# Kernel tuning notes

Measured on AMD Instinct MI355X. Metric: run time of the kernel, lower is better.

## Reference

```python
import jax, jax.numpy as jnp
import numpy as np

N, E, D = 100000, 1600000, 128      # nodes, edges, in_channels = MLP out_dim
L = 3                               # num GIN layers
OC = D + L * D                      # concat width = 512
CH, CHID = 4, 256                   # num ChannelMLPs, their hidden dim


def setup_inputs() -> dict:
    key = jax.random.key(0)
    ks = jax.random.split(key, 10)
    s = lambda fan_in: 1.0 / np.sqrt(fan_in)
    x = jax.random.normal(ks[0], (N, D), dtype=jnp.float32)
    edge_index = jax.random.randint(ks[1], (2, E), 0, N, dtype=jnp.int32)
    # conv MLPs: per layer 3 linear layers (in->hid, hid->hid, hid->out), all 128x128
    convW = jax.random.normal(ks[2], (L, 3, D, D), dtype=jnp.float32) * s(D)
    convB = jnp.zeros((L, 3, D), dtype=jnp.float32)
    # channel MLPs: 512 -> 256 -> 256 -> 1, ReLU after every layer (output_activation='relu')
    chanW1 = jax.random.normal(ks[3], (CH, OC, CHID), dtype=jnp.float32) * s(OC)
    chanB1 = jnp.zeros((CH, CHID), dtype=jnp.float32)
    chanW2 = jax.random.normal(ks[4], (CH, CHID, CHID), dtype=jnp.float32) * s(CHID)
    chanB2 = jnp.zeros((CH, CHID), dtype=jnp.float32)
    chanW3 = jax.random.normal(ks[5], (CH, CHID, 1), dtype=jnp.float32) * s(CHID)
    chanB3 = jnp.zeros((CH, 1), dtype=jnp.float32)
    return {"x": x, "edge_index": edge_index, "convW": convW, "convB": convB,
            "chanW1": chanW1, "chanB1": chanB1, "chanW2": chanW2, "chanB2": chanB2,
            "chanW3": chanW3, "chanB3": chanB3}


def reference(x, edge_index, convW, convB, chanW1, chanB1, chanW2, chanB2, chanW3, chanB3):
    src, dst = edge_index[0], edge_index[1]
    n = x.shape[0]
    feats = [x]                      # skip_first_features=False -> keep input
    h = x
    for l in range(L):
        # GINConv, eps=0: mlp((1+eps)*h + sum_{j in N(i)} h_j)
        agg = jax.ops.segment_sum(h[src], dst, num_segments=n)  # scatter-add at targets
        h = h + agg
        for k in range(3):           # MLP: Lin+ReLU x3 (2 hidden + relu output activation)
            h = jax.nn.relu(h @ convW[l, k] + convB[l, k])
        feats.append(h)
    xcat = jnp.concatenate(feats, axis=1)                       # [N, 512]
    # channel MLPs vectorized over the channel axis c
    h1 = jax.nn.relu(jnp.einsum('nd,cdh->cnh', xcat, chanW1) + chanB1[:, None, :])
    h2 = jax.nn.relu(jnp.einsum('cnh,chk->cnk', h1, chanW2) + chanB2[:, None, :])
    h3 = jax.nn.relu(jnp.einsum('cnh,cho->cno', h2, chanW3) + chanB3[:, None, :])
    return jnp.transpose(h3[..., 0])                            # [N, num_ChannelMLPs]
```

## Files before the change

### kernel.cpp

```cpp
#include <hip/hip_runtime.h>
#include <hip/hip_bf16.h>

#define D 128
#define NLAYER 3
#define NCH 4

typedef __attribute__((ext_vector_type(8))) short short8;
typedef __attribute__((ext_vector_type(4))) float f32x4;

__device__ __forceinline__ ushort f2bf(float f) {
    unsigned int u = __builtin_bit_cast(unsigned int, f);
    u += 0x7fffu + ((u >> 16) & 1u);
    return (ushort)(u >> 16);
}
__device__ __forceinline__ float bflo(unsigned int u) {
    return __builtin_bit_cast(float, u << 16);
}
__device__ __forceinline__ float bfhi(unsigned int u) {
    return __builtin_bit_cast(float, u & 0xffff0000u);
}

__global__ void hist_kernel(const int* __restrict__ dst, int* __restrict__ deg, int E) {
    int e = blockIdx.x * 256 + threadIdx.x;
    if (e < E) atomicAdd(&deg[dst[e]], 1);
}

__global__ __launch_bounds__(256) void blocksum_kernel(
    const int* __restrict__ deg, int* __restrict__ bsum, int n)
{
    int i = blockIdx.x * 256 + threadIdx.x;
    int v = (i < n) ? deg[i] : 0;
#pragma unroll
    for (int o = 1; o < 64; o <<= 1) v += __shfl_xor(v, o);
    __shared__ int s[4];
    if ((threadIdx.x & 63) == 0) s[threadIdx.x >> 6] = v;
    __syncthreads();
    if (threadIdx.x == 0) bsum[blockIdx.x] = s[0] + s[1] + s[2] + s[3];
}

__global__ __launch_bounds__(512) void scanblk_kernel(
    const int* __restrict__ bsum, int* __restrict__ boff, int nb,
    int* __restrict__ offs, int n, int E)
{
    __shared__ int sh[512];
    int t = threadIdx.x;
    sh[t] = (t < nb) ? bsum[t] : 0;
    __syncthreads();
    for (int d = 1; d < 512; d <<= 1) {
        int v = (t >= d) ? sh[t - d] : 0;
        __syncthreads();
        sh[t] += v;
        __syncthreads();
    }
    if (t < nb) boff[t] = (t == 0) ? 0 : sh[t - 1];
    if (t == 0) offs[n] = E;
}

__global__ __launch_bounds__(256) void blockscan_kernel(
    const int* __restrict__ deg, const int* __restrict__ boff,
    int* __restrict__ offs, int* __restrict__ cursor, int n)
{
    __shared__ int sh[256];
    int t = threadIdx.x;
    int i = blockIdx.x * 256 + t;
    int v = (i < n) ? deg[i] : 0;
    sh[t] = v;
    __syncthreads();
    for (int d = 1; d < 256; d <<= 1) {
        int u = (t >= d) ? sh[t - d] : 0;
        __syncthreads();
        sh[t] += u;
        __syncthreads();
    }
    if (i < n) {
        int ex = boff[blockIdx.x] + sh[t] - v;
        offs[i] = ex; cursor[i] = ex;
    }
}

#define FILL_CHUNK 4096
__global__ __launch_bounds__(256) void fill_part_kernel(
    const int* __restrict__ src, const int* __restrict__ dst,
    int* __restrict__ cursor, int* __restrict__ csr,
    int E, int nPer, int N)
{
    int cls = blockIdx.x & 7;
    int base = (blockIdx.x >> 3) * FILL_CHUNK;
    int lo = cls * nPer;
    int hi = lo + nPer; if (hi > N) hi = N;
    int end = base + FILL_CHUNK; if (end > E) end = E;
    for (int e = base + threadIdx.x; e < end; e += 256) {
        int d = dst[e];
        int s = src[e];
        if (d >= lo && d < hi) {
            int p = atomicAdd(&cursor[d], 1);
            csr[p] = s;
        }
    }
}

__global__ __launch_bounds__(256) void cvtx_kernel(
    const float* __restrict__ x, ushort* __restrict__ xb, int total8)
{
    int i = blockIdx.x * 256 + threadIdx.x;
    if (i >= total8) return;
    const float* gp = x + (size_t)i * 8;
    float4 v0 = *(const float4*)gp;
    float4 v1 = *(const float4*)(gp + 4);
    short8 pk;
    pk[0] = (short)f2bf(v0.x); pk[1] = (short)f2bf(v0.y);
    pk[2] = (short)f2bf(v0.z); pk[3] = (short)f2bf(v0.w);
    pk[4] = (short)f2bf(v1.x); pk[5] = (short)f2bf(v1.y);
    pk[6] = (short)f2bf(v1.z); pk[7] = (short)f2bf(v1.w);
    *(short8*)(xb + (size_t)i * 8) = pk;
}

__global__ void cvtW_kernel(const float* __restrict__ W, ushort* __restrict__ Wt,
                            int K, int Ncols) {
    __shared__ float tile[32][33];
    int c = blockIdx.z;
    int k0 = blockIdx.x * 32, n0 = blockIdx.y * 32;
    const float* Wc = W + (size_t)c * K * Ncols;
    ushort* Wtc = Wt + (size_t)c * K * Ncols;
    int tx = threadIdx.x & 31, ty = threadIdx.x >> 5;
#pragma unroll
    for (int i = 0; i < 4; ++i) {
        int k = k0 + ty + i * 8;
        tile[ty + i * 8][tx] = Wc[(size_t)k * Ncols + n0 + tx];
    }
    __syncthreads();
#pragma unroll
    for (int i = 0; i < 4; ++i) {
        int n = n0 + ty + i * 8;
        Wtc[(size_t)n * K + k0 + tx] = f2bf(tile[tx][ty + i * 8]);
    }
}

__global__ __launch_bounds__(256) void agg_bf16(
    const ushort* __restrict__ h,
    const int* __restrict__ offs, const int* __restrict__ csr,
    ushort* __restrict__ outb, int n)
{
    int wid = (blockIdx.x * 256 + threadIdx.x) >> 6;
    int lane = threadIdx.x & 63;
    if (wid >= n) return;
    const unsigned int* hb = (const unsigned int*)h;
    unsigned int u = hb[(size_t)wid * 64 + lane];
    float ax = bflo(u), ay = bfhi(u);
    int b = offs[wid], e = offs[wid + 1];
    int j = b;
    for (; j + 4 <= e; j += 4) {
        int s0 = csr[j], s1 = csr[j + 1], s2 = csr[j + 2], s3 = csr[j + 3];
        unsigned int u0 = hb[(size_t)s0 * 64 + lane];
        unsigned int u1 = hb[(size_t)s1 * 64 + lane];
        unsigned int u2 = hb[(size_t)s2 * 64 + lane];
        unsigned int u3 = hb[(size_t)s3 * 64 + lane];
        ax += (bflo(u0) + bflo(u1)) + (bflo(u2) + bflo(u3));
        ay += (bfhi(u0) + bfhi(u1)) + (bfhi(u2) + bfhi(u3));
    }
    for (; j < e; ++j) {
        unsigned int u0 = hb[(size_t)csr[j] * 64 + lane];
        ax += bflo(u0); ay += bfhi(u0);
    }
    unsigned int po = (unsigned int)f2bf(ax) | ((unsigned int)f2bf(ay) << 16);
    ((unsigned int*)outb)[(size_t)wid * 64 + lane] = po;
}

__global__ __launch_bounds__(256) void gin_mlp_mfma(
    const ushort* __restrict__ A,
    const ushort* __restrict__ WtL,
    const float* __restrict__ biasL,
    ushort* __restrict__ Out,
    int nrows)
{
    __shared__ __align__(16) ushort As[128 * 128];
    __shared__ __align__(16) ushort Bs[128 * 128];
    const int t = threadIdx.x;
    const int w = t >> 6, lane = t & 63;
    const int quad = lane >> 4, c15 = lane & 15;
    const int wr = w >> 1, wc = w & 1;
    const int rowbase = blockIdx.x * 128;

#pragma unroll
    for (int i = 0; i < 8; ++i) {
        int lin = (i * 4 + w) * 64 + lane;
        int row = lin >> 4, slot = lin & 15, g = slot ^ (row & 15);
        int grow = rowbase + row;
        if (grow >= nrows) grow = 0;
        const ushort* gp = A + (size_t)grow * 128 + g * 8;
        __builtin_amdgcn_global_load_lds(
            (const __attribute__((address_space(1))) void*)gp,
            (__attribute__((address_space(3))) void*)&As[(i * 4 + w) * 512],
            16, 0, 0);
    }
#pragma unroll
    for (int i = 0; i < 8; ++i) {
        int lin = (i * 4 + w) * 64 + lane;
        int n = lin >> 4, slot = lin & 15, g = slot ^ (n & 15);
        const ushort* gp = WtL + (size_t)n * 128 + g * 8;
        __builtin_amdgcn_global_load_lds(
            (const __attribute__((address_space(1))) void*)gp,
            (__attribute__((address_space(3))) void*)&Bs[(i * 4 + w) * 512],
            16, 0, 0);
    }
    __syncthreads();

    for (int s = 0; s < 3; ++s) {
        f32x4 acc[4][4];
#pragma unroll
        for (int i = 0; i < 4; ++i)
#pragma unroll
            for (int j = 0; j < 4; ++j)
#pragma unroll
                for (int r = 0; r < 4; ++r) acc[i][j][r] = 0.f;

#pragma unroll
        for (int ks = 0; ks < 4; ++ks) {
            short8 af[4], bf[4];
#pragma unroll
            for (int tr = 0; tr < 4; ++tr) {
                int r = wr * 64 + tr * 16 + c15;
                af[tr] = *(const short8*)&As[r * 128 + (((ks * 4 + quad) ^ (r & 15)) * 8)];
            }
#pragma unroll
            for (int tc = 0; tc < 4; ++tc) {
                int n = wc * 64 + tc * 16 + c15;
                bf[tc] = *(const short8*)&Bs[n * 128 + (((ks * 4 + quad) ^ (n & 15)) * 8)];
            }
#pragma unroll
            for (int tr = 0; tr < 4; ++tr)
#pragma unroll
                for (int tc = 0; tc < 4; ++tc)
                    acc[tr][tc] = __builtin_amdgcn_mfma_f32_16x16x32_bf16(
                        af[tr], bf[tc], acc[tr][tc], 0, 0, 0);
        }
        __syncthreads();

        if (s < 2) {
#pragma unroll
            for (int tc = 0; tc < 4; ++tc) {
                int col = wc * 64 + tc * 16 + c15;
                float bv = biasL[s * 128 + col];
#pragma unroll
                for (int tr = 0; tr < 4; ++tr)
#pragma unroll
                    for (int rg = 0; rg < 4; ++rg) {
                        int row = wr * 64 + tr * 16 + quad * 4 + rg;
                        As[row * 128 + (((col >> 3) ^ (row & 15)) * 8) + (col & 7)]
                            = f2bf(fmaxf(acc[tr][tc][rg] + bv, 0.f));
                    }
            }
            const ushort* Wn = WtL + (size_t)(s + 1) * 128 * 128;
#pragma unroll
            for (int i = 0; i < 8; ++i) {
                int lin = (i * 4 + w) * 64 + lane;
                int n = lin >> 4, slot = lin & 15, g = slot ^ (n & 15);
                const ushort* gp = Wn + (size_t)n * 128 + g * 8;
                __builtin_amdgcn_global_load_lds(
                    (const __attribute__((address_space(1))) void*)gp,
                    (__attribute__((address_space(3))) void*)&Bs[(i * 4 + w) * 512],
                    16, 0, 0);
            }
            __syncthreads();
        } else {
#pragma unroll
            for (int tc = 0; tc < 4; ++tc) {
                int col = wc * 64 + tc * 16 + c15;
                float bv = biasL[2 * 128 + col];
#pragma unroll
                for (int tr = 0; tr < 4; ++tr)
#pragma unroll
                    for (int rg = 0; rg < 4; ++rg) {
                        int grow = rowbase + wr * 64 + tr * 16 + quad * 4 + rg;
                        if (grow < nrows)
                            Out[(size_t)grow * 128 + col]
                                = f2bf(fmaxf(acc[tr][tc][rg] + bv, 0.f));
                    }
            }
        }
    }
}

__global__ __launch_bounds__(256, 2) void chan_l1_mfma(
    const ushort* __restrict__ A0, const ushort* __restrict__ A1,
    const ushort* __restrict__ A2, const ushort* __restrict__ A3,
    const ushort* __restrict__ WtAll,
    const float* __restrict__ b1all,
    ushort* __restrict__ T1,
    int r0, int rows, int N)
{
    __shared__ __align__(16) ushort As[128 * 64];
    __shared__ __align__(16) ushort Bs[256 * 64];
    const int t = threadIdx.x;
    const int w = t >> 6, lane = t & 63;
    const int quad = lane >> 4, c15 = lane & 15;
    const int wr = w >> 1, wc = w & 1;
    const int rowbase = blockIdx.x * 128;
    const int colbase = blockIdx.y * 256;
    const ushort* Asrc[4] = {A0, A1, A2, A3};

    f32x4 acc[4][8];
#pragma unroll
    for (int i = 0; i < 4; ++i)
#pragma unroll
        for (int j = 0; j < 8; ++j)
#pragma unroll
            for (int r = 0; r < 4; ++r) acc[i][j][r] = 0.f;

    for (int kc = 0; kc < 512; kc += 64) {
        const ushort* Ab = Asrc[kc >> 7];
        const int within = kc & 127;
#pragma unroll
        for (int i = 0; i < 4; ++i) {
            int lin = (i * 4 + w) * 64 + lane;
            int row = lin >> 3, slot = lin & 7, g = slot ^ (row & 7);
            int grow = r0 + rowbase + row;
            if (grow >= N) grow = r0;
            const ushort* gp = Ab + (size_t)grow * 128 + within + g * 8;
            __builtin_amdgcn_global_load_lds(
                (const __attribute__((address_space(1))) void*)gp,
                (__attribute__((address_space(3))) void*)&As[(i * 4 + w) * 512],
                16, 0, 0);
        }
#pragma unroll
        for (int i = 0; i < 8; ++i) {
            int lin = (i * 4 + w) * 64 + lane;
            int n = lin >> 3, slot = lin & 7, g = slot ^ (n & 7);
            const ushort* gp = WtAll + (size_t)(colbase + n) * 512 + kc + g * 8;
            __builtin_amdgcn_global_load_lds(
                (const __attribute__((address_space(1))) void*)gp,
                (__attribute__((address_space(3))) void*)&Bs[(i * 4 + w) * 512],
                16, 0, 0);
        }
        __syncthreads();
#pragma unroll
        for (int ks = 0; ks < 2; ++ks) {
            const int K8 = ks * 4;
            short8 af[4], bf[8];
#pragma unroll
            for (int tr = 0; tr < 4; ++tr) {
                int r = wr * 64 + tr * 16 + c15;
                af[tr] = *(const short8*)&As[r * 64 + (((K8 + quad) ^ (r & 7)) * 8)];
            }
#pragma unroll
            for (int tc = 0; tc < 8; ++tc) {
                int n = wc * 128 + tc * 16 + c15;
                bf[tc] = *(const short8*)&Bs[n * 64 + (((K8 + quad) ^ (n & 7)) * 8)];
            }
#pragma unroll
            for (int tr = 0; tr < 4; ++tr)
#pragma unroll
                for (int tc = 0; tc < 8; ++tc)
                    acc[tr][tc] = __builtin_amdgcn_mfma_f32_16x16x32_bf16(
                        af[tr], bf[tc], acc[tr][tc], 0, 0, 0);
        }
        __syncthreads();
    }

#pragma unroll
    for (int tc = 0; tc < 8; ++tc) {
        int col = colbase + wc * 128 + tc * 16 + c15;
        float bias = b1all[col];
#pragma unroll
        for (int tr = 0; tr < 4; ++tr)
#pragma unroll
            for (int rg = 0; rg < 4; ++rg) {
                int lrow = rowbase + wr * 64 + tr * 16 + quad * 4 + rg;
                if (lrow < rows)
                    T1[(size_t)lrow * 1024 + col] = f2bf(fmaxf(acc[tr][tc][rg] + bias, 0.f));
            }
    }
}

__global__ __launch_bounds__(256) void chan_l23_mfma(
    const ushort* __restrict__ T1c,
    const ushort* __restrict__ Wt2,
    const float* __restrict__ b2,
    const float* __restrict__ w3,
    const float* __restrict__ b3,
    float* __restrict__ out,
    int r0, int rows, int c)
{
    __shared__ __align__(16) ushort As[64 * 64];
    __shared__ __align__(16) ushort Bs[256 * 64];
    __shared__ float red[64][4];
    const int t = threadIdx.x;
    const int w = t >> 6, lane = t & 63;
    const int quad = lane >> 4, c15 = lane & 15;
    const int rowbase = blockIdx.x * 64;

    f32x4 acc[4][4];
#pragma unroll
    for (int i = 0; i < 4; ++i)
#pragma unroll
        for (int j = 0; j < 4; ++j)
#pragma unroll
            for (int r = 0; r < 4; ++r) acc[i][j][r] = 0.f;

    for (int kc = 0; kc < 256; kc += 64) {
#pragma unroll
        for (int i = 0; i < 2; ++i) {
            int lin = (i * 4 + w) * 64 + lane;
            int row = lin >> 3, slot = lin & 7, g = slot ^ (row & 7);
            int lrow = rowbase + row;
            if (lrow >= rows) lrow = 0;
            const ushort* gp = T1c + (size_t)lrow * 1024 + kc + g * 8;
            __builtin_amdgcn_global_load_lds(
                (const __attribute__((address_space(1))) void*)gp,
                (__attribute__((address_space(3))) void*)&As[(i * 4 + w) * 512],
                16, 0, 0);
        }
#pragma unroll
        for (int i = 0; i < 8; ++i) {
            int lin = (i * 4 + w) * 64 + lane;
            int n = lin >> 3, slot = lin & 7, g = slot ^ (n & 7);
            const ushort* gp = Wt2 + (size_t)n * 256 + kc + g * 8;
            __builtin_amdgcn_global_load_lds(
                (const __attribute__((address_space(1))) void*)gp,
                (__attribute__((address_space(3))) void*)&Bs[(i * 4 + w) * 512],
                16, 0, 0);
        }
        __syncthreads();
#pragma unroll
        for (int ks = 0; ks < 2; ++ks) {
            const int K8 = ks * 4;
            short8 af[4], bf[4];
#pragma unroll
            for (int tr = 0; tr < 4; ++tr) {
                int r = tr * 16 + c15;
                af[tr] = *(const short8*)&As[r * 64 + (((K8 + quad) ^ (r & 7)) * 8)];
            }
#pragma unroll
            for (int tc = 0; tc < 4; ++tc) {
                int n = w * 64 + tc * 16 + c15;
                bf[tc] = *(const short8*)&Bs[n * 64 + (((K8 + quad) ^ (n & 7)) * 8)];
            }
#pragma unroll
            for (int tr = 0; tr < 4; ++tr)
#pragma unroll
                for (int tc = 0; tc < 4; ++tc)
                    acc[tr][tc] = __builtin_amdgcn_mfma_f32_16x16x32_bf16(
                        af[tr], bf[tc], acc[tr][tc], 0, 0, 0);
        }
        __syncthreads();
    }

    float b2v[4], w3v[4];
#pragma unroll
    for (int tc = 0; tc < 4; ++tc) {
        int col = w * 64 + tc * 16 + c15;
        b2v[tc] = b2[col];
        w3v[tc] = w3[col];
    }
#pragma unroll
    for (int tr = 0; tr < 4; ++tr)
#pragma unroll
        for (int rg = 0; rg < 4; ++rg) {
            float p = 0.f;
#pragma unroll
            for (int tc = 0; tc < 4; ++tc)
                p += fmaxf(acc[tr][tc][rg] + b2v[tc], 0.f) * w3v[tc];
            p += __shfl_xor(p, 1);
            p += __shfl_xor(p, 2);
            p += __shfl_xor(p, 4);
            p += __shfl_xor(p, 8);
            if (c15 == 0) red[tr * 16 + quad * 4 + rg][w] = p;
        }
    __syncthreads();
    if (t < 64) {
        int lrow = rowbase + t;
        if (lrow < rows) {
            float s = red[t][0] + red[t][1] + red[t][2] + red[t][3] + b3[0];
            out[(size_t)(r0 + lrow) * NCH + c] = fmaxf(s, 0.f);
        }
    }
}

extern "C" void kernel_launch(void* const* d_in, const int* in_sizes, int n_in,
                              void* d_out, int out_size, void* d_ws, size_t ws_size,
                              hipStream_t stream) {
    const float* x        = (const float*)d_in[0];
    const int*   eidx     = (const int*)d_in[1];
    const float* convW    = (const float*)d_in[2];
    const float* convB    = (const float*)d_in[3];
    const float* chanW1   = (const float*)d_in[4];
    const float* chanB1   = (const float*)d_in[5];
    const float* chanW2   = (const float*)d_in[6];
    const float* chanB2   = (const float*)d_in[7];
    const float* chanW3   = (const float*)d_in[8];
    const float* chanB3   = (const float*)d_in[9];
    float* out = (float*)d_out;

    const int N = in_sizes[0] / D;
    const int E = in_sizes[1] / 2;
    const int* srcp = eidx;
    const int* dstp = eidx + E;
    const int nb = (N + 255) / 256;

    char* w = (char*)d_ws;
    auto take = [&](size_t bytes) {
        char* p = w;
        w += (bytes + 255) & ~(size_t)255;
        return p;
    };
    ushort* xb     = (ushort*)take((size_t)N * D * 2);
    ushort* h0     = (ushort*)take((size_t)N * D * 2);
    ushort* h1     = (ushort*)take((size_t)N * D * 2);
    ushort* h2     = (ushort*)take((size_t)N * D * 2);
    int*    deg    = (int*)take((size_t)N * 4);
    int*    offs   = (int*)take((size_t)(N + 1) * 4);
    int*    cursor = (int*)take((size_t)N * 4);
    int*    bsum   = (int*)take((size_t)nb * 4);
    int*    boff   = (int*)take((size_t)nb * 4);
    ushort* Wt1b   = (ushort*)take((size_t)NCH * 256 * 512 * 2);
    ushort* Wt2b   = (ushort*)take((size_t)NCH * 256 * 256 * 2);
    ushort* WtC    = (ushort*)take((size_t)NLAYER * 3 * D * D * 2);

    size_t used = (size_t)(w - (char*)d_ws);
    if (used > ws_size) return;
    size_t rem = ws_size - used;
    size_t need_gin = (((size_t)E * 4 + 255) & ~(size_t)255) + (size_t)N * D * 2;
    if (rem < need_gin || rem < (size_t)128 * 2048) return;

    int*    csr = (int*)w;
    ushort* a   = (ushort*)(w + (((size_t)E * 4 + 255) & ~(size_t)255));
    ushort* t1  = (ushort*)w;
    long rcap = (long)(rem / 2048);
    int R = (int)((rcap / 128) * 128);
    const int Nup = ((N + 127) / 128) * 128;
    if (R > Nup) R = Nup;

    hipMemsetAsync(deg, 0, (size_t)N * 4, stream);
    hist_kernel<<<(E + 255) / 256, 256, 0, stream>>>(dstp, deg, E);
    blocksum_kernel<<<nb, 256, 0, stream>>>(deg, bsum, N);
    scanblk_kernel<<<1, 512, 0, stream>>>(bsum, boff, nb, offs, N, E);
    blockscan_kernel<<<nb, 256, 0, stream>>>(deg, boff, offs, cursor, N);
    {
        int nchunks = (E + FILL_CHUNK - 1) / FILL_CHUNK;
        int nPer = (N + 7) / 8;
        fill_part_kernel<<<nchunks * 8, 256, 0, stream>>>(
            srcp, dstp, cursor, csr, E, nPer, N);
    }

    cvtx_kernel<<<(N * 16 + 255) / 256, 256, 0, stream>>>(x, xb, N * 16);
    cvtW_kernel<<<dim3(512 / 32, 256 / 32, NCH), 256, 0, stream>>>(chanW1, Wt1b, 512, 256);
    cvtW_kernel<<<dim3(256 / 32, 256 / 32, NCH), 256, 0, stream>>>(chanW2, Wt2b, 256, 256);
    cvtW_kernel<<<dim3(D / 32, D / 32, NLAYER * 3), 256, 0, stream>>>(convW, WtC, D, D);

    const int rowtiles = (N + 127) / 128;
    const int aggblocks = (N * 64 + 255) / 256;

    ushort* hbuf[NLAYER] = {h0, h1, h2};
    const ushort* prev = xb;
    for (int l = 0; l < NLAYER; ++l) {
        agg_bf16<<<aggblocks, 256, 0, stream>>>(prev, offs, csr, a, N);
        gin_mlp_mfma<<<rowtiles, 256, 0, stream>>>(
            a, WtC + (size_t)l * 3 * D * D, convB + (size_t)l * 3 * D, hbuf[l], N);
        prev = hbuf[l];
    }

    for (int r0 = 0; r0 < N; r0 += R) {
        int rows = N - r0; if (rows > R) rows = R;
        int rt128 = (rows + 127) / 128;
        int rt64  = (rows + 63) / 64;
        chan_l1_mfma<<<dim3(rt128, 4), 256, 0, stream>>>(
            xb, h0, h1, h2, Wt1b, chanB1, t1, r0, rows, N);
        for (int c = 0; c < NCH; ++c) {
            chan_l23_mfma<<<rt64, 256, 0, stream>>>(
                t1 + (size_t)c * 256,
                Wt2b + (size_t)c * 256 * 256,
                chanB2 + (size_t)c * 256,
                chanW3 + (size_t)c * 256,
                chanB3 + c,
                out, r0, rows, c);
        }
    }
}
```

Measured before the change: 983.1 us.

## Fuse channel MLP layers 1-3 into one kernel keeping hidden tile in LDS

Merges the first channel-MLP GEMM with the second and third layers into a single kernel per (64-row tile, channel). The 256-wide hidden activation is kept in a swizzled LDS buffer instead of being written to and re-read from a global T1 scratch array, and the row-chunking loop goes away. The cost is a smaller 64-row tile for layer 1, so W1 is re-fetched more often per row, and more LDS per block, which may limit occupancy.

```diff
diff --git a/kernel.cpp b/kernel.cpp
--- a/kernel.cpp
+++ b/kernel.cpp
@@ -281,29 +281,36 @@
     }
 }
 
-__global__ __launch_bounds__(256, 2) void chan_l1_mfma(
+__global__ __launch_bounds__(256, 2) void chan_fused_mfma(
     const ushort* __restrict__ A0, const ushort* __restrict__ A1,
     const ushort* __restrict__ A2, const ushort* __restrict__ A3,
-    const ushort* __restrict__ WtAll,
-    const float* __restrict__ b1all,
-    ushort* __restrict__ T1,
-    int r0, int rows, int N)
-{
-    __shared__ __align__(16) ushort As[128 * 64];
+    const ushort* __restrict__ Wt1,
+    const float* __restrict__ b1,
+    const ushort* __restrict__ Wt2,
+    const float* __restrict__ b2,
+    const float* __restrict__ w3,
+    const float* __restrict__ b3,
+    float* __restrict__ out,
+    int N)
+{
+    __shared__ __align__(16) ushort As[64 * 64];
     __shared__ __align__(16) ushort Bs[256 * 64];
+    __shared__ __align__(16) ushort Ts[64 * 256];
+    __shared__ float red[64][4];
     const int t = threadIdx.x;
     const int w = t >> 6, lane = t & 63;
     const int quad = lane >> 4, c15 = lane & 15;
-    const int wr = w >> 1, wc = w & 1;
-    const int rowbase = blockIdx.x * 128;
-    const int colbase = blockIdx.y * 256;
+    const int rowbase = blockIdx.x * 64;
+    const int c = blockIdx.y;
     const ushort* Asrc[4] = {A0, A1, A2, A3};
-
-    f32x4 acc[4][8];
+    const ushort* W1c = Wt1 + (size_t)c * 256 * 512;
+    const ushort* W2c = Wt2 + (size_t)c * 256 * 256;
+
+    f32x4 acc[4][4];
 #pragma unroll
     for (int i = 0; i < 4; ++i)
 #pragma unroll
-        for (int j = 0; j < 8; ++j)
+        for (int j = 0; j < 4; ++j)
 #pragma unroll
             for (int r = 0; r < 4; ++r) acc[i][j][r] = 0.f;
 
@@ -311,11 +318,11 @@
         const ushort* Ab = Asrc[kc >> 7];
         const int within = kc & 127;
 #pragma unroll
-        for (int i = 0; i < 4; ++i) {
+        for (int i = 0; i < 2; ++i) {
             int lin = (i * 4 + w) * 64 + lane;
             int row = lin >> 3, slot = lin & 7, g = slot ^ (row & 7);
-            int grow = r0 + rowbase + row;
-            if (grow >= N) grow = r0;
+            int grow = rowbase + row;
+            if (grow >= N) grow = 0;
             const ushort* gp = Ab + (size_t)grow * 128 + within + g * 8;
             __builtin_amdgcn_global_load_lds(
                 (const __attribute__((address_space(1))) void*)gp,
@@ -326,7 +333,7 @@
         for (int i = 0; i < 8; ++i) {
             int lin = (i * 4 + w) * 64 + lane;
             int n = lin >> 3, slot = lin & 7, g = slot ^ (n & 7);
-            const ushort* gp = WtAll + (size_t)(colbase + n) * 512 + kc + g * 8;
+            const ushort* gp = W1c + (size_t)n * 512 + kc + g * 8;
             __builtin_amdgcn_global_load_lds(
                 (const __attribute__((address_space(1))) void*)gp,
                 (__attribute__((address_space(3))) void*)&Bs[(i * 4 + w) * 512],
@@ -336,21 +343,21 @@
 #pragma unroll
         for (int ks = 0; ks < 2; ++ks) {
             const int K8 = ks * 4;
-            short8 af[4], bf[8];
+            short8 af[4], bf[4];
 #pragma unroll
             for (int tr = 0; tr < 4; ++tr) {
-                int r = wr * 64 + tr * 16 + c15;
+                int r = tr * 16 + c15;
                 af[tr] = *(const short8*)&As[r * 64 + (((K8 + quad) ^ (r & 7)) * 8)];
             }
 #pragma unroll
-            for (int tc = 0; tc < 8; ++tc) {
-                int n = wc * 128 + tc * 16 + c15;
+            for (int tc = 0; tc < 4; ++tc) {
+                int n = w * 64 + tc * 16 + c15;
                 bf[tc] = *(const short8*)&Bs[n * 64 + (((K8 + quad) ^ (n & 7)) * 8)];
             }
 #pragma unroll
             for (int tr = 0; tr < 4; ++tr)
 #pragma unroll
-                for (int tc = 0; tc < 8; ++tc)
+                for (int tc = 0; tc < 4; ++tc)
                     acc[tr][tc] = __builtin_amdgcn_mfma_f32_16x16x32_bf16(
                         af[tr], bf[tc], acc[tr][tc], 0, 0, 0);
         }
@@ -358,38 +365,20 @@
     }
 
 #pragma unroll
-    for (int tc = 0; tc < 8; ++tc) {
-        int col = colbase + wc * 128 + tc * 16 + c15;
-        float bias = b1all[col];
+    for (int tc = 0; tc < 4; ++tc) {
+        int col = w * 64 + tc * 16 + c15;
+        float bv = b1[c * 256 + col];
 #pragma unroll
         for (int tr = 0; tr < 4; ++tr)
 #pragma unroll
             for (int rg = 0; rg < 4; ++rg) {
-                int lrow = rowbase + wr * 64 + tr * 16 + quad * 4 + rg;
-                if (lrow < rows)
-                    T1[(size_t)lrow * 1024 + col] = f2bf(fmaxf(acc[tr][tc][rg] + bias, 0.f));
-            }
-    }
-}
-
-__global__ __launch_bounds__(256) void chan_l23_mfma(
-    const ushort* __restrict__ T1c,
-    const ushort* __restrict__ Wt2,
-    const float* __restrict__ b2,
-    const float* __restrict__ w3,
-    const float* __restrict__ b3,
-    float* __restrict__ out,
-    int r0, int rows, int c)
-{
-    __shared__ __align__(16) ushort As[64 * 64];
-    __shared__ __align__(16) ushort Bs[256 * 64];
-    __shared__ float red[64][4];
-    const int t = threadIdx.x;
-    const int w = t >> 6, lane = t & 63;
-    const int quad = lane >> 4, c15 = lane & 15;
-    const int rowbase = blockIdx.x * 64;
-
-    f32x4 acc[4][4];
+                int row = tr * 16 + quad * 4 + rg;
+                Ts[row * 256 + (((col >> 3) ^ (row & 31)) * 8) + (col & 7)]
+                    = f2bf(fmaxf(acc[tr][tc][rg] + bv, 0.f));
+            }
+    }
+    __syncthreads();
+
 #pragma unroll
     for (int i = 0; i < 4; ++i)
 #pragma unroll
@@ -398,23 +387,11 @@
             for (int r = 0; r < 4; ++r) acc[i][j][r] = 0.f;
 
     for (int kc = 0; kc < 256; kc += 64) {
-#pragma unroll
-        for (int i = 0; i < 2; ++i) {
-            int lin = (i * 4 + w) * 64 + lane;
-            int row = lin >> 3, slot = lin & 7, g = slot ^ (row & 7);
-            int lrow = rowbase + row;
-            if (lrow >= rows) lrow = 0;
-            const ushort* gp = T1c + (size_t)lrow * 1024 + kc + g * 8;
-            __builtin_amdgcn_global_load_lds(
-                (const __attribute__((address_space(1))) void*)gp,
-                (__attribute__((address_space(3))) void*)&As[(i * 4 + w) * 512],
-                16, 0, 0);
-        }
 #pragma unroll
         for (int i = 0; i < 8; ++i) {
             int lin = (i * 4 + w) * 64 + lane;
             int n = lin >> 3, slot = lin & 7, g = slot ^ (n & 7);
-            const ushort* gp = Wt2 + (size_t)n * 256 + kc + g * 8;
+            const ushort* gp = W2c + (size_t)n * 256 + kc + g * 8;
             __builtin_amdgcn_global_load_lds(
                 (const __attribute__((address_space(1))) void*)gp,
                 (__attribute__((address_space(3))) void*)&Bs[(i * 4 + w) * 512],
@@ -423,17 +400,17 @@
         __syncthreads();
 #pragma unroll
         for (int ks = 0; ks < 2; ++ks) {
-            const int K8 = ks * 4;
             short8 af[4], bf[4];
+            const int g0 = (kc >> 3) + ks * 4 + quad;
 #pragma unroll
             for (int tr = 0; tr < 4; ++tr) {
                 int r = tr * 16 + c15;
-                af[tr] = *(const short8*)&As[r * 64 + (((K8 + quad) ^ (r & 7)) * 8)];
+                af[tr] = *(const short8*)&Ts[r * 256 + ((g0 ^ (r & 31)) * 8)];
             }
 #pragma unroll
             for (int tc = 0; tc < 4; ++tc) {
                 int n = w * 64 + tc * 16 + c15;
-                bf[tc] = *(const short8*)&Bs[n * 64 + (((K8 + quad) ^ (n & 7)) * 8)];
+                bf[tc] = *(const short8*)&Bs[n * 64 + ((((ks * 4) + quad) ^ (n & 7)) * 8)];
             }
 #pragma unroll
             for (int tr = 0; tr < 4; ++tr)
@@ -449,8 +426,8 @@
 #pragma unroll
     for (int tc = 0; tc < 4; ++tc) {
         int col = w * 64 + tc * 16 + c15;
-        b2v[tc] = b2[col];
-        w3v[tc] = w3[col];
+        b2v[tc] = b2[c * 256 + col];
+        w3v[tc] = w3[c * 256 + col];
     }
 #pragma unroll
     for (int tr = 0; tr < 4; ++tr)
@@ -468,10 +445,10 @@
         }
     __syncthreads();
     if (t < 64) {
-        int lrow = rowbase + t;
-        if (lrow < rows) {
-            float s = red[t][0] + red[t][1] + red[t][2] + red[t][3] + b3[0];
-            out[(size_t)(r0 + lrow) * NCH + c] = fmaxf(s, 0.f);
+        int grow = rowbase + t;
+        if (grow < N) {
+            float s = red[t][0] + red[t][1] + red[t][2] + red[t][3] + b3[c];
+            out[(size_t)grow * NCH + c] = fmaxf(s, 0.f);
         }
     }
 }
@@ -520,15 +497,10 @@
     if (used > ws_size) return;
     size_t rem = ws_size - used;
     size_t need_gin = (((size_t)E * 4 + 255) & ~(size_t)255) + (size_t)N * D * 2;
-    if (rem < need_gin || rem < (size_t)128 * 2048) return;
+    if (rem < need_gin) return;
 
     int*    csr = (int*)w;
     ushort* a   = (ushort*)(w + (((size_t)E * 4 + 255) & ~(size_t)255));
-    ushort* t1  = (ushort*)w;
-    long rcap = (long)(rem / 2048);
-    int R = (int)((rcap / 128) * 128);
-    const int Nup = ((N + 127) / 128) * 128;
-    if (R > Nup) R = Nup;
 
     hipMemsetAsync(deg, 0, (size_t)N * 4, stream);
     hist_kernel<<<(E + 255) / 256, 256, 0, stream>>>(dstp, deg, E);
@@ -559,20 +531,9 @@
         prev = hbuf[l];
     }
 
-    for (int r0 = 0; r0 < N; r0 += R) {
-        int rows = N - r0; if (rows > R) rows = R;
-        int rt128 = (rows + 127) / 128;
-        int rt64  = (rows + 63) / 64;
-        chan_l1_mfma<<<dim3(rt128, 4), 256, 0, stream>>>(
-            xb, h0, h1, h2, Wt1b, chanB1, t1, r0, rows, N);
-        for (int c = 0; c < NCH; ++c) {
-            chan_l23_mfma<<<rt64, 256, 0, stream>>>(
-                t1 + (size_t)c * 256,
-                Wt2b + (size_t)c * 256 * 256,
-                chanB2 + (size_t)c * 256,
-                chanW3 + (size_t)c * 256,
-                chanB3 + c,
-                out, r0, rows, c);
-        }
-    }
-}
+    const int rt64 = (N + 63) / 64;
+    chan_fused_mfma<<<dim3(rt64, NCH), 256, 0, stream>>>(
+        xb, h0, h1, h2,
+        Wt1b, chanB1, Wt2b, chanB2, chanW3, chanB3,
+        out, N);
+}
```

Result: faster. 868.5 us (-11.7%).
